# Kernel optimization log

Measured on AMD Instinct MI355X. Metric: run time of the kernel, lower is better.

Reference implementation:

```python
import jax, jax.numpy as jnp
import numpy as np

B = 65536
IN = 32 * 8      # input_size * n_dim
H = 256          # joint_hidden_size


def setup_inputs() -> dict:
    key = jax.random.key(0)
    ks = jax.random.split(key, 8)
    joint_h = jax.random.normal(ks[0], (B, H), dtype=jnp.float32)
    mgn_h = jax.random.normal(ks[1], (B, IN), dtype=jnp.float32)
    # xavier-uniform scale for W, plain normal for U (orthogonal in torch; any
    # dense matrix is fine for a numerical reference), zeros for biases.
    w_lim = float(np.sqrt(6.0 / (IN + H)))
    W_r = jax.random.uniform(ks[2], (IN, H), jnp.float32, -w_lim, w_lim)
    W_z = jax.random.uniform(ks[3], (IN, H), jnp.float32, -w_lim, w_lim)
    W_h = jax.random.uniform(ks[4], (IN, H), jnp.float32, -w_lim, w_lim)
    U_r = jax.random.normal(ks[5], (H, H), jnp.float32) / np.float32(np.sqrt(H))
    U_z = jax.random.normal(ks[6], (H, H), jnp.float32) / np.float32(np.sqrt(H))
    U_h = jax.random.normal(ks[7], (H, H), jnp.float32) / np.float32(np.sqrt(H))
    b_r = jnp.zeros((H,), jnp.float32)
    b_z = jnp.zeros((H,), jnp.float32)
    b_h = jnp.zeros((H,), jnp.float32)
    return {"joint_h": joint_h, "mgn_h": mgn_h,
            "W_r": W_r, "W_z": W_z, "W_h": W_h,
            "U_r": U_r, "U_z": U_z, "U_h": U_h,
            "b_r": b_r, "b_z": b_z, "b_h": b_h}


def reference(joint_h, mgn_h, W_r, W_z, W_h, U_r, U_z, U_h, b_r, b_z, b_h):
    # fuse the three input GEMMs and the two non-gated hidden GEMMs by
    # concatenating weights (same math as 6 separate mm's)
    W = jnp.concatenate([W_r, W_z, W_h], axis=1)        # [IN, 3H]
    U_rz = jnp.concatenate([U_r, U_z], axis=1)          # [H, 2H]
    x_proj = mgn_h @ W                                  # [B, 3H]
    h_proj = joint_h @ U_rz                             # [B, 2H]
    Hd = joint_h.shape[1]
    r = jax.nn.sigmoid(x_proj[:, :Hd] + h_proj[:, :Hd] + b_r)
    z = jax.nn.sigmoid(x_proj[:, Hd:2 * Hd] + h_proj[:, Hd:] + b_z)
    h_tilde = jnp.tanh(x_proj[:, 2 * Hd:] + (joint_h * r) @ U_h + b_h)
    return h_tilde + z * (joint_h - h_tilde)
```

## Files before the change

### kernel.cpp

```cpp
#include <hip/hip_runtime.h>

#define H     256
#define BM    128
#define NTHR  512
#define LDK2  264

typedef __attribute__((ext_vector_type(4))) float f32x4;
typedef __attribute__((ext_vector_type(8))) short bf16x8;

__device__ __forceinline__ ushort f2bf(float f) {
    union { float f; unsigned u; } v; v.f = f;
    unsigned u = v.u;
    unsigned r = (u + 0x7fffu + ((u >> 16) & 1u)) >> 16;
    return (ushort)r;
}
__device__ __forceinline__ float bf2f(ushort h) {
    union { unsigned u; float f; } v; v.u = ((unsigned)h) << 16;
    return v.f;
}
__device__ __forceinline__ float sigmoid_f(float x) {
    return __builtin_amdgcn_rcpf(1.0f + __expf(-x));
}
__device__ __forceinline__ float tanh_f(float x) {
    float ax = fabsf(x);
    float e  = __expf(-2.0f * ax);
    float t  = (1.0f - e) * __builtin_amdgcn_rcpf(1.0f + e);
    return copysignf(t, x);
}

__global__ void prep_w(const float* __restrict__ Wr, const float* __restrict__ Wz,
                       const float* __restrict__ Wh, const float* __restrict__ Ur,
                       const float* __restrict__ Uz, const float* __restrict__ Uh,
                       ushort* __restrict__ P)
{
    const int k  = blockIdx.x;
    const int kk = k & 255;
    const bool hi = k >= 256;
    for (int n = threadIdx.x; n < 768; n += 256) {
        float v;
        if (n < 256)      v = (hi ? Ur : Wr)[kk * 256 + n];
        else if (n < 512) v = (hi ? Uz : Wz)[kk * 256 + (n - 256)];
        else              v = (hi ? Uh : Wh)[kk * 256 + (n - 512)];
        P[(size_t)n * 512 + k] = f2bf(v);
    }
}

#define MFMA(a, b, c) __builtin_amdgcn_mfma_f32_16x16x32_bf16((a), (b), (c), 0, 0, 0)

#define RZ_STEP(SB, KOFF, K0) do {                                            \
    bf16x8 bR_[2], bZ_[2], af_[8];                                            \
    _Pragma("unroll") for (int j_ = 0; j_ < 2; ++j_) {                        \
        bR_[j_] = *(const bf16x8*)(pBr + (size_t)j_ * 16 * 512 + (KOFF) + (K0)); \
        bZ_[j_] = *(const bf16x8*)(pBz + (size_t)j_ * 16 * 512 + (KOFF) + (K0)); \
    }                                                                         \
    _Pragma("unroll") for (int i_ = 0; i_ < 8; ++i_)                          \
        af_[i_] = *(const bf16x8*)&SB[(i_ * 16 + l15) * LDK2 + (K0) + kq * 8];\
    _Pragma("unroll") for (int j_ = 0; j_ < 2; ++j_)                          \
    _Pragma("unroll") for (int i_ = 0; i_ < 8; ++i_) {                        \
        aR[i_][j_] = MFMA(af_[i_], bR_[j_], aR[i_][j_]);                      \
        aZ[i_][j_] = MFMA(af_[i_], bZ_[j_], aZ[i_][j_]);                      \
    }                                                                         \
} while (0)

#define H_STEP(SB, KOFF, K0) do {                                             \
    bf16x8 bH_[2], af_[8];                                                    \
    _Pragma("unroll") for (int j_ = 0; j_ < 2; ++j_)                          \
        bH_[j_] = *(const bf16x8*)(pBh + (size_t)j_ * 16 * 512 + (KOFF) + (K0)); \
    _Pragma("unroll") for (int i_ = 0; i_ < 8; ++i_)                          \
        af_[i_] = *(const bf16x8*)&SB[(i_ * 16 + l15) * LDK2 + (K0) + kq * 8];\
    _Pragma("unroll") for (int j_ = 0; j_ < 2; ++j_)                          \
    _Pragma("unroll") for (int i_ = 0; i_ < 8; ++i_)                          \
        aH[i_][j_] = MFMA(af_[i_], bH_[j_], aH[i_][j_]);                      \
} while (0)

#define LOADJ(JV, CI) do {                                                    \
    _Pragma("unroll") for (int i_ = 0; i_ < 4; ++i_) {                        \
        const int c_ = tid + ((CI) * 4 + i_) * NTHR;                          \
        JV[i_] = *(const f32x4*)(joint + (r0 + (c_ >> 6)) * H + (c_ & 63) * 4); \
    }                                                                         \
} while (0)

#define COMMITJ(JV, CI) do {                                                  \
    _Pragma("unroll") for (int i_ = 0; i_ < 4; ++i_) {                        \
        const int c_ = tid + ((CI) * 4 + i_) * NTHR;                          \
        ushort4 w_;                                                           \
        w_.x = f2bf(JV[i_][0]); w_.y = f2bf(JV[i_][1]);                       \
        w_.z = f2bf(JV[i_][2]); w_.w = f2bf(JV[i_][3]);                       \
        *(ushort4*)&sb1[(c_ >> 6) * LDK2 + (c_ & 63) * 4] = w_;               \
    }                                                                         \
} while (0)

__global__ __launch_bounds__(NTHR, 2)
void gru_main(const float* __restrict__ joint, const float* __restrict__ mgn,
              const ushort* __restrict__ P,
              const float* __restrict__ br_, const float* __restrict__ bz_,
              const float* __restrict__ bh_, float* __restrict__ out)
{
    __shared__ ushort sb0[BM * LDK2];
    __shared__ ushort sb1[BM * LDK2];

    const int tid  = threadIdx.x;
    const int wave = tid >> 6;
    const int lane = tid & 63;
    const int l15  = lane & 15;
    const int kq   = lane >> 4;
    const int colbase = wave * 32;
    const size_t r0 = (size_t)blockIdx.x * BM;

    const ushort* __restrict__ pBr = P + (size_t)(colbase + l15) * 512 + kq * 8;
    const ushort* __restrict__ pBz = pBr + (size_t)256 * 512;
    const ushort* __restrict__ pBh = pBr + (size_t)512 * 512;

    #pragma unroll
    for (int i = 0; i < 16; ++i) {
        const int c   = tid + i * NTHR;
        const int row = c >> 6;
        const int c4  = (c & 63) * 4;
        const f32x4 v = *(const f32x4*)(mgn + (r0 + row) * H + c4);
        ushort4 w;
        w.x = f2bf(v[0]); w.y = f2bf(v[1]); w.z = f2bf(v[2]); w.w = f2bf(v[3]);
        *(ushort4*)&sb0[row * LDK2 + c4] = w;
    }
    __syncthreads();

    f32x4 aR[8][2], aZ[8][2];
    #pragma unroll
    for (int i = 0; i < 8; ++i)
        #pragma unroll
        for (int j = 0; j < 2; ++j) {
            aR[i][j] = (f32x4){0.f, 0.f, 0.f, 0.f};
            aZ[i][j] = (f32x4){0.f, 0.f, 0.f, 0.f};
        }

    {
        f32x4 jvA[4], jvB[4];
        LOADJ(jvA, 0);
        RZ_STEP(sb0, 0, 0);   RZ_STEP(sb0, 0, 32);
        LOADJ(jvB, 1);
        RZ_STEP(sb0, 0, 64);  RZ_STEP(sb0, 0, 96);
        COMMITJ(jvA, 0); LOADJ(jvA, 2);
        RZ_STEP(sb0, 0, 128); RZ_STEP(sb0, 0, 160);
        COMMITJ(jvB, 1); LOADJ(jvB, 3);
        RZ_STEP(sb0, 0, 192); RZ_STEP(sb0, 0, 224);
        COMMITJ(jvA, 2);
        COMMITJ(jvB, 3);
    }
    __syncthreads();

    #pragma unroll 4
    for (int k0 = 0; k0 < 256; k0 += 32) RZ_STEP(sb1, 256, k0);
    __syncthreads();

    float br[2], bz[2], bh[2];
    #pragma unroll
    for (int j = 0; j < 2; ++j) {
        const int c = colbase + j * 16 + l15;
        br[j] = br_[c]; bz[j] = bz_[c]; bh[j] = bh_[c];
    }
    #pragma unroll
    for (int i = 0; i < 8; ++i)
        #pragma unroll
        for (int j = 0; j < 2; ++j)
            #pragma unroll
            for (int q = 0; q < 4; ++q) {
                const int row = i * 16 + kq * 4 + q;
                const int c   = colbase + j * 16 + l15;
                const float r = sigmoid_f(aR[i][j][q] + br[j]);
                const float hj = bf2f(sb1[row * LDK2 + c]);
                sb1[row * LDK2 + c] = f2bf(hj * r);
                aZ[i][j][q] = sigmoid_f(aZ[i][j][q] + bz[j]);
            }
    __syncthreads();

    f32x4 aH[8][2];
    #pragma unroll
    for (int i = 0; i < 8; ++i)
        #pragma unroll
        for (int j = 0; j < 2; ++j)
            aH[i][j] = (f32x4){0.f, 0.f, 0.f, 0.f};

    #pragma unroll 4
    for (int k0 = 0; k0 < 256; k0 += 32) H_STEP(sb1, 256, k0);
    #pragma unroll 4
    for (int k0 = 0; k0 < 256; k0 += 32) H_STEP(sb0, 0, k0);

    #pragma unroll
    for (int i = 0; i < 8; ++i)
        #pragma unroll
        for (int j = 0; j < 2; ++j)
            #pragma unroll
            for (int q = 0; q < 4; ++q) {
                const int row = i * 16 + kq * 4 + q;
                const int c   = colbase + j * 16 + l15;
                const float ht = tanh_f(aH[i][j][q] + bh[j]);
                const float z  = aZ[i][j][q];
                const float h  = joint[(r0 + row) * H + c];
                out[(r0 + row) * H + c] = ht + z * (h - ht);
            }
}

extern "C" void kernel_launch(void* const* d_in, const int* in_sizes, int n_in,
                              void* d_out, int out_size, void* d_ws, size_t ws_size,
                              hipStream_t stream)
{
    const float* joint = (const float*)d_in[0];
    const float* mgn   = (const float*)d_in[1];
    const float* Wr    = (const float*)d_in[2];
    const float* Wz    = (const float*)d_in[3];
    const float* Wh    = (const float*)d_in[4];
    const float* Ur    = (const float*)d_in[5];
    const float* Uz    = (const float*)d_in[6];
    const float* Uh    = (const float*)d_in[7];
    const float* br    = (const float*)d_in[8];
    const float* bz    = (const float*)d_in[9];
    const float* bh    = (const float*)d_in[10];

    ushort* P  = (ushort*)d_ws;
    float* out = (float*)d_out;

    prep_w<<<512, 256, 0, stream>>>(Wr, Wz, Wh, Ur, Uz, Uh, P);

    const int nrows = 65536;
    gru_main<<<nrows / BM, NTHR, 0, stream>>>(joint, mgn, P, br, bz, bh, out);
}
```

Measured before the change: 105.3 us.

## Split block into 16 waves with 2D row/column wave tiling

Doubles the block to 1024 threads and splits the 128-row tile across two wave groups of 64 rows each. Each wave now holds half as many accumulators, which lowers register pressure and gives more waves per CU to hide latency. In exchange, each B fragment fetched from global/L2 is reused over fewer MFMAs, so per-block weight traffic doubles. Larger blocks also make synchronisation coarser.

Result: slower. 137.3 us (+30.3%).

```diff
diff --git a/kernel.cpp b/kernel.cpp
--- a/kernel.cpp
+++ b/kernel.cpp
@@ -2,7 +2,7 @@
 
 #define H     256
 #define BM    128
-#define NTHR  512
+#define NTHR  1024
 #define LDK2  264
 
 typedef __attribute__((ext_vector_type(4))) float f32x4;
@@ -47,42 +47,50 @@
 
 #define MFMA(a, b, c) __builtin_amdgcn_mfma_f32_16x16x32_bf16((a), (b), (c), 0, 0, 0)
 
-#define RZ_STEP(SB, KOFF, K0) do {                                            \
-    bf16x8 bR_[2], bZ_[2], af_[8];                                            \
-    _Pragma("unroll") for (int j_ = 0; j_ < 2; ++j_) {                        \
-        bR_[j_] = *(const bf16x8*)(pBr + (size_t)j_ * 16 * 512 + (KOFF) + (K0)); \
-        bZ_[j_] = *(const bf16x8*)(pBz + (size_t)j_ * 16 * 512 + (KOFF) + (K0)); \
-    }                                                                         \
-    _Pragma("unroll") for (int i_ = 0; i_ < 8; ++i_)                          \
-        af_[i_] = *(const bf16x8*)&SB[(i_ * 16 + l15) * LDK2 + (K0) + kq * 8];\
-    _Pragma("unroll") for (int j_ = 0; j_ < 2; ++j_)                          \
-    _Pragma("unroll") for (int i_ = 0; i_ < 8; ++i_) {                        \
-        aR[i_][j_] = MFMA(af_[i_], bR_[j_], aR[i_][j_]);                      \
-        aZ[i_][j_] = MFMA(af_[i_], bZ_[j_], aZ[i_][j_]);                      \
-    }                                                                         \
-} while (0)
-
-#define H_STEP(SB, KOFF, K0) do {                                             \
-    bf16x8 bH_[2], af_[8];                                                    \
-    _Pragma("unroll") for (int j_ = 0; j_ < 2; ++j_)                          \
-        bH_[j_] = *(const bf16x8*)(pBh + (size_t)j_ * 16 * 512 + (KOFF) + (K0)); \
-    _Pragma("unroll") for (int i_ = 0; i_ < 8; ++i_)                          \
-        af_[i_] = *(const bf16x8*)&SB[(i_ * 16 + l15) * LDK2 + (K0) + kq * 8];\
-    _Pragma("unroll") for (int j_ = 0; j_ < 2; ++j_)                          \
-    _Pragma("unroll") for (int i_ = 0; i_ < 8; ++i_)                          \
-        aH[i_][j_] = MFMA(af_[i_], bH_[j_], aH[i_][j_]);                      \
+#define RZ_STEP(SB, K0, KOFF) do {                                            \
+    bf16x8 bR_[2], bZ_[2];                                                    \
+    bR_[0] = *(const bf16x8*)(pBr + (KOFF) + (K0));                           \
+    bR_[1] = *(const bf16x8*)(pBr + (size_t)16 * 512 + (KOFF) + (K0));        \
+    bZ_[0] = *(const bf16x8*)(pBz + (KOFF) + (K0));                           \
+    bZ_[1] = *(const bf16x8*)(pBz + (size_t)16 * 512 + (KOFF) + (K0));        \
+    _Pragma("unroll") for (int ip_ = 0; ip_ < 2; ++ip_) {                     \
+        bf16x8 a0_ = *(const bf16x8*)&SB[(rowbase + (ip_ * 2 + 0) * 16 + l15) * LDK2 + (K0) + kq * 8]; \
+        bf16x8 a1_ = *(const bf16x8*)&SB[(rowbase + (ip_ * 2 + 1) * 16 + l15) * LDK2 + (K0) + kq * 8]; \
+        aR[ip_ * 2 + 0][0] = MFMA(a0_, bR_[0], aR[ip_ * 2 + 0][0]);           \
+        aR[ip_ * 2 + 1][0] = MFMA(a1_, bR_[0], aR[ip_ * 2 + 1][0]);           \
+        aZ[ip_ * 2 + 0][0] = MFMA(a0_, bZ_[0], aZ[ip_ * 2 + 0][0]);           \
+        aZ[ip_ * 2 + 1][0] = MFMA(a1_, bZ_[0], aZ[ip_ * 2 + 1][0]);           \
+        aR[ip_ * 2 + 0][1] = MFMA(a0_, bR_[1], aR[ip_ * 2 + 0][1]);           \
+        aR[ip_ * 2 + 1][1] = MFMA(a1_, bR_[1], aR[ip_ * 2 + 1][1]);           \
+        aZ[ip_ * 2 + 0][1] = MFMA(a0_, bZ_[1], aZ[ip_ * 2 + 0][1]);           \
+        aZ[ip_ * 2 + 1][1] = MFMA(a1_, bZ_[1], aZ[ip_ * 2 + 1][1]);           \
+    }                                                                         \
+} while (0)
+
+#define H_STEP(SB, K0, KOFF) do {                                             \
+    bf16x8 bH_[2];                                                            \
+    bH_[0] = *(const bf16x8*)(pBh + (KOFF) + (K0));                           \
+    bH_[1] = *(const bf16x8*)(pBh + (size_t)16 * 512 + (KOFF) + (K0));        \
+    _Pragma("unroll") for (int ip_ = 0; ip_ < 2; ++ip_) {                     \
+        bf16x8 a0_ = *(const bf16x8*)&SB[(rowbase + (ip_ * 2 + 0) * 16 + l15) * LDK2 + (K0) + kq * 8]; \
+        bf16x8 a1_ = *(const bf16x8*)&SB[(rowbase + (ip_ * 2 + 1) * 16 + l15) * LDK2 + (K0) + kq * 8]; \
+        aH[ip_ * 2 + 0][0] = MFMA(a0_, bH_[0], aH[ip_ * 2 + 0][0]);           \
+        aH[ip_ * 2 + 1][0] = MFMA(a1_, bH_[0], aH[ip_ * 2 + 1][0]);           \
+        aH[ip_ * 2 + 0][1] = MFMA(a0_, bH_[1], aH[ip_ * 2 + 0][1]);           \
+        aH[ip_ * 2 + 1][1] = MFMA(a1_, bH_[1], aH[ip_ * 2 + 1][1]);           \
+    }                                                                         \
 } while (0)
 
 #define LOADJ(JV, CI) do {                                                    \
-    _Pragma("unroll") for (int i_ = 0; i_ < 4; ++i_) {                        \
-        const int c_ = tid + ((CI) * 4 + i_) * NTHR;                          \
+    _Pragma("unroll") for (int i_ = 0; i_ < 2; ++i_) {                        \
+        const int c_ = tid + ((CI) * 2 + i_) * NTHR;                          \
         JV[i_] = *(const f32x4*)(joint + (r0 + (c_ >> 6)) * H + (c_ & 63) * 4); \
     }                                                                         \
 } while (0)
 
 #define COMMITJ(JV, CI) do {                                                  \
-    _Pragma("unroll") for (int i_ = 0; i_ < 4; ++i_) {                        \
-        const int c_ = tid + ((CI) * 4 + i_) * NTHR;                          \
+    _Pragma("unroll") for (int i_ = 0; i_ < 2; ++i_) {                        \
+        const int c_ = tid + ((CI) * 2 + i_) * NTHR;                          \
         ushort4 w_;                                                           \
         w_.x = f2bf(JV[i_][0]); w_.y = f2bf(JV[i_][1]);                       \
         w_.z = f2bf(JV[i_][2]); w_.w = f2bf(JV[i_][3]);                       \
@@ -90,7 +98,7 @@
     }                                                                         \
 } while (0)
 
-__global__ __launch_bounds__(NTHR, 2)
+__global__ __launch_bounds__(NTHR, 4)
 void gru_main(const float* __restrict__ joint, const float* __restrict__ mgn,
               const ushort* __restrict__ P,
               const float* __restrict__ br_, const float* __restrict__ bz_,
@@ -104,7 +112,8 @@
     const int lane = tid & 63;
     const int l15  = lane & 15;
     const int kq   = lane >> 4;
-    const int colbase = wave * 32;
+    const int rowbase = (wave >> 3) * 64;
+    const int colbase = (wave & 7) * 32;
     const size_t r0 = (size_t)blockIdx.x * BM;
 
     const ushort* __restrict__ pBr = P + (size_t)(colbase + l15) * 512 + kq * 8;
@@ -112,7 +121,7 @@
     const ushort* __restrict__ pBh = pBr + (size_t)512 * 512;
 
     #pragma unroll
-    for (int i = 0; i < 16; ++i) {
+    for (int i = 0; i < 8; ++i) {
         const int c   = tid + i * NTHR;
         const int row = c >> 6;
         const int c4  = (c & 63) * 4;
@@ -123,9 +132,9 @@
     }
     __syncthreads();
 
-    f32x4 aR[8][2], aZ[8][2];
+    f32x4 aR[4][2], aZ[4][2];
     #pragma unroll
-    for (int i = 0; i < 8; ++i)
+    for (int i = 0; i < 4; ++i)
         #pragma unroll
         for (int j = 0; j < 2; ++j) {
             aR[i][j] = (f32x4){0.f, 0.f, 0.f, 0.f};
@@ -133,70 +142,76 @@
         }
 
     {
-        f32x4 jvA[4], jvB[4];
-        LOADJ(jvA, 0);
-        RZ_STEP(sb0, 0, 0);   RZ_STEP(sb0, 0, 32);
-        LOADJ(jvB, 1);
-        RZ_STEP(sb0, 0, 64);  RZ_STEP(sb0, 0, 96);
-        COMMITJ(jvA, 0); LOADJ(jvA, 2);
-        RZ_STEP(sb0, 0, 128); RZ_STEP(sb0, 0, 160);
-        COMMITJ(jvB, 1); LOADJ(jvB, 3);
-        RZ_STEP(sb0, 0, 192); RZ_STEP(sb0, 0, 224);
-        COMMITJ(jvA, 2);
-        COMMITJ(jvB, 3);
-    }
-    __syncthreads();
-
-    #pragma unroll 4
-    for (int k0 = 0; k0 < 256; k0 += 32) RZ_STEP(sb1, 256, k0);
-    __syncthreads();
-
-    float br[2], bz[2], bh[2];
+        f32x4 jv[2];
+        LOADJ(jv, 0);
+        RZ_STEP(sb0, 0, 0);   RZ_STEP(sb0, 32, 0);
+        COMMITJ(jv, 0);  LOADJ(jv, 1);
+        RZ_STEP(sb0, 64, 0);  RZ_STEP(sb0, 96, 0);
+        COMMITJ(jv, 1);  LOADJ(jv, 2);
+        RZ_STEP(sb0, 128, 0); RZ_STEP(sb0, 160, 0);
+        COMMITJ(jv, 2);  LOADJ(jv, 3);
+        RZ_STEP(sb0, 192, 0); RZ_STEP(sb0, 224, 0);
+        COMMITJ(jv, 3);
+    }
+    __syncthreads();
+
+    #pragma unroll 2
+    for (int k0 = 0; k0 < 256; k0 += 32) RZ_STEP(sb1, k0, 256);
+    __syncthreads();
+
+    {
+        float br[2], bz[2];
+        #pragma unroll
+        for (int j = 0; j < 2; ++j) {
+            const int c = colbase + j * 16 + l15;
+            br[j] = br_[c]; bz[j] = bz_[c];
+        }
+        #pragma unroll
+        for (int i = 0; i < 4; ++i)
+            #pragma unroll
+            for (int j = 0; j < 2; ++j)
+                #pragma unroll
+                for (int q = 0; q < 4; ++q) {
+                    const int row = rowbase + i * 16 + kq * 4 + q;
+                    const int c   = colbase + j * 16 + l15;
+                    const float r = sigmoid_f(aR[i][j][q] + br[j]);
+                    const float hj = bf2f(sb1[row * LDK2 + c]);
+                    sb1[row * LDK2 + c] = f2bf(hj * r);
+                    aZ[i][j][q] = sigmoid_f(aZ[i][j][q] + bz[j]);
+                }
+    }
+    __syncthreads();
+
+    f32x4 aH[4][2];
     #pragma unroll
-    for (int j = 0; j < 2; ++j) {
-        const int c = colbase + j * 16 + l15;
-        br[j] = br_[c]; bz[j] = bz_[c]; bh[j] = bh_[c];
-    }
-    #pragma unroll
-    for (int i = 0; i < 8; ++i)
-        #pragma unroll
-        for (int j = 0; j < 2; ++j)
-            #pragma unroll
-            for (int q = 0; q < 4; ++q) {
-                const int row = i * 16 + kq * 4 + q;
-                const int c   = colbase + j * 16 + l15;
-                const float r = sigmoid_f(aR[i][j][q] + br[j]);
-                const float hj = bf2f(sb1[row * LDK2 + c]);
-                sb1[row * LDK2 + c] = f2bf(hj * r);
-                aZ[i][j][q] = sigmoid_f(aZ[i][j][q] + bz[j]);
-            }
-    __syncthreads();
-
-    f32x4 aH[8][2];
-    #pragma unroll
-    for (int i = 0; i < 8; ++i)
+    for (int i = 0; i < 4; ++i)
         #pragma unroll
         for (int j = 0; j < 2; ++j)
             aH[i][j] = (f32x4){0.f, 0.f, 0.f, 0.f};
 
-    #pragma unroll 4
-    for (int k0 = 0; k0 < 256; k0 += 32) H_STEP(sb1, 256, k0);
-    #pragma unroll 4
-    for (int k0 = 0; k0 < 256; k0 += 32) H_STEP(sb0, 0, k0);
-
-    #pragma unroll
-    for (int i = 0; i < 8; ++i)
-        #pragma unroll
-        for (int j = 0; j < 2; ++j)
+    #pragma unroll 2
+    for (int k0 = 0; k0 < 256; k0 += 32) H_STEP(sb1, k0, 256);
+    #pragma unroll 2
+    for (int k0 = 0; k0 < 256; k0 += 32) H_STEP(sb0, k0, 0);
+
+    {
+        float bh[2];
+        #pragma unroll
+        for (int j = 0; j < 2; ++j) bh[j] = bh_[colbase + j * 16 + l15];
+        #pragma unroll
+        for (int i = 0; i < 4; ++i)
             #pragma unroll
-            for (int q = 0; q < 4; ++q) {
-                const int row = i * 16 + kq * 4 + q;
-                const int c   = colbase + j * 16 + l15;
-                const float ht = tanh_f(aH[i][j][q] + bh[j]);
-                const float z  = aZ[i][j][q];
-                const float h  = joint[(r0 + row) * H + c];
-                out[(r0 + row) * H + c] = ht + z * (h - ht);
-            }
+            for (int j = 0; j < 2; ++j)
+                #pragma unroll
+                for (int q = 0; q < 4; ++q) {
+                    const int row = rowbase + i * 16 + kq * 4 + q;
+                    const int c   = colbase + j * 16 + l15;
+                    const float ht = tanh_f(aH[i][j][q] + bh[j]);
+                    const float z  = aZ[i][j][q];
+                    const float h  = joint[(r0 + row) * H + c];
+                    out[(r0 + row) * H + c] = ht + z * (h - ht);
+                }
+    }
 }
 
 extern "C" void kernel_launch(void* const* d_in, const int* in_sizes, int n_in,
```

## Switch GRU kernel to 32x32 MFMA with pipelined staging and register-cached h,z

Applied to the files above, without the earlier changes.

Replaces the 16x16x32 bf16 MFMA tiling with 32x32x16 bf16 MFMA, so each wave covers 128 rows by 32 columns with fewer, larger fragments. It also streams the mgn tile into LDS in stages overlapped with the first r/z GEMM steps, and software-pipelines the B-operand global loads four steps ahead. The bf16 hidden state and z gate are packed into registers, which removes the global re-read of joint in the epilogue. The costs are higher register pressure, extra barriers between staging chunks, and using the bf16-rounded h in the final blend, which reduces accuracy.

After: 91.61 us. 1.15x faster.

```diff
diff --git a/kernel.cpp b/kernel.cpp
--- a/kernel.cpp
+++ b/kernel.cpp
@@ -5,8 +5,9 @@
 #define NTHR  512
 #define LDK2  264
 
-typedef __attribute__((ext_vector_type(4))) float f32x4;
-typedef __attribute__((ext_vector_type(8))) short bf16x8;
+typedef __attribute__((ext_vector_type(4)))  float f32x4;
+typedef __attribute__((ext_vector_type(16))) float f32x16;
+typedef __attribute__((ext_vector_type(8)))  short bf16x8;
 
 __device__ __forceinline__ ushort f2bf(float f) {
     union { float f; unsigned u; } v; v.f = f;
@@ -45,47 +46,69 @@
     }
 }
 
-#define MFMA(a, b, c) __builtin_amdgcn_mfma_f32_16x16x32_bf16((a), (b), (c), 0, 0, 0)
-
-#define RZ_STEP(SB, KOFF, K0) do {                                            \
-    bf16x8 bR_[2], bZ_[2], af_[8];                                            \
-    _Pragma("unroll") for (int j_ = 0; j_ < 2; ++j_) {                        \
-        bR_[j_] = *(const bf16x8*)(pBr + (size_t)j_ * 16 * 512 + (KOFF) + (K0)); \
-        bZ_[j_] = *(const bf16x8*)(pBz + (size_t)j_ * 16 * 512 + (KOFF) + (K0)); \
-    }                                                                         \
-    _Pragma("unroll") for (int i_ = 0; i_ < 8; ++i_)                          \
-        af_[i_] = *(const bf16x8*)&SB[(i_ * 16 + l15) * LDK2 + (K0) + kq * 8];\
-    _Pragma("unroll") for (int j_ = 0; j_ < 2; ++j_)                          \
-    _Pragma("unroll") for (int i_ = 0; i_ < 8; ++i_) {                        \
-        aR[i_][j_] = MFMA(af_[i_], bR_[j_], aR[i_][j_]);                      \
-        aZ[i_][j_] = MFMA(af_[i_], bZ_[j_], aZ[i_][j_]);                      \
-    }                                                                         \
-} while (0)
-
-#define H_STEP(SB, KOFF, K0) do {                                             \
-    bf16x8 bH_[2], af_[8];                                                    \
-    _Pragma("unroll") for (int j_ = 0; j_ < 2; ++j_)                          \
-        bH_[j_] = *(const bf16x8*)(pBh + (size_t)j_ * 16 * 512 + (KOFF) + (K0)); \
-    _Pragma("unroll") for (int i_ = 0; i_ < 8; ++i_)                          \
-        af_[i_] = *(const bf16x8*)&SB[(i_ * 16 + l15) * LDK2 + (K0) + kq * 8];\
-    _Pragma("unroll") for (int j_ = 0; j_ < 2; ++j_)                          \
-    _Pragma("unroll") for (int i_ = 0; i_ < 8; ++i_)                          \
-        aH[i_][j_] = MFMA(af_[i_], bH_[j_], aH[i_][j_]);                      \
-} while (0)
-
-#define LOADJ(JV, CI) do {                                                    \
-    _Pragma("unroll") for (int i_ = 0; i_ < 4; ++i_) {                        \
-        const int c_ = tid + ((CI) * 4 + i_) * NTHR;                          \
-        JV[i_] = *(const f32x4*)(joint + (r0 + (c_ >> 6)) * H + (c_ & 63) * 4); \
-    }                                                                         \
-} while (0)
-
-#define COMMITJ(JV, CI) do {                                                  \
-    _Pragma("unroll") for (int i_ = 0; i_ < 4; ++i_) {                        \
-        const int c_ = tid + ((CI) * 4 + i_) * NTHR;                          \
+#define MFMA32(a, b, c) __builtin_amdgcn_mfma_f32_32x32x16_bf16((a), (b), (c), 0, 0, 0)
+
+#define LBRZ(B, BR, BZ) do {                                                  \
+    const int ko_ = ((B) < 16) ? (B) * 16 : 256 + ((B) - 16) * 16;            \
+    BR = *(const bf16x8*)(pBr + ko_);                                         \
+    BZ = *(const bf16x8*)(pBz + ko_);                                         \
+} while (0)
+
+#define LBH(B, BH) do {                                                       \
+    const int ko_ = ((B) < 16) ? 256 + (B) * 16 : ((B) - 16) * 16;            \
+    BH = *(const bf16x8*)(pBh + ko_);                                         \
+} while (0)
+
+#define STEP1(SB, S16, BR, BZ) do {                                           \
+    const int kk_ = (S16) * 16;                                               \
+    bf16x8 af_[4];                                                            \
+    _Pragma("unroll") for (int rf_ = 0; rf_ < 4; ++rf_)                       \
+        af_[rf_] = *(const bf16x8*)&SB[(rf_ * 32 + l31) * LDK2 + kk_ + hi8];  \
+    _Pragma("unroll") for (int rf_ = 0; rf_ < 4; ++rf_) {                     \
+        aR[rf_] = MFMA32(af_[rf_], BR, aR[rf_]);                              \
+        aZ[rf_] = MFMA32(af_[rf_], BZ, aZ[rf_]);                              \
+    }                                                                         \
+} while (0)
+
+#define STEP2(SB, S16, BH) do {                                               \
+    const int kk_ = (S16) * 16;                                               \
+    bf16x8 af_[4];                                                            \
+    _Pragma("unroll") for (int rf_ = 0; rf_ < 4; ++rf_)                       \
+        af_[rf_] = *(const bf16x8*)&SB[(rf_ * 32 + l31) * LDK2 + kk_ + hi8];  \
+    _Pragma("unroll") for (int rf_ = 0; rf_ < 4; ++rf_)                       \
+        aH[rf_] = MFMA32(af_[rf_], BH, aH[rf_]);                              \
+} while (0)
+
+#define SLOADM(S) do {                                                        \
+    _Pragma("unroll") for (int j_ = 0; j_ < 4; ++j_) {                        \
+        const int u_ = j_ * NTHR + tid;                                       \
+        mv[j_] = *(const f32x4*)(mgn + (r0 + (u_ >> 4)) * H + ((S) * 16 + (u_ & 15)) * 4); \
+    }                                                                         \
+} while (0)
+
+#define SCOMMITM(S) do {                                                      \
+    _Pragma("unroll") for (int j_ = 0; j_ < 4; ++j_) {                        \
+        const int u_ = j_ * NTHR + tid;                                       \
         ushort4 w_;                                                           \
-        w_.x = f2bf(JV[i_][0]); w_.y = f2bf(JV[i_][1]);                       \
-        w_.z = f2bf(JV[i_][2]); w_.w = f2bf(JV[i_][3]);                       \
+        w_.x = f2bf(mv[j_][0]); w_.y = f2bf(mv[j_][1]);                       \
+        w_.z = f2bf(mv[j_][2]); w_.w = f2bf(mv[j_][3]);                       \
+        *(ushort4*)&sb0[(u_ >> 4) * LDK2 + ((S) * 16 + (u_ & 15)) * 4] = w_;  \
+    }                                                                         \
+} while (0)
+
+#define LOADJ(C) do {                                                         \
+    _Pragma("unroll") for (int i_ = 0; i_ < 2; ++i_) {                        \
+        const int c_ = tid + ((C) * 2 + i_) * NTHR;                           \
+        jv[i_] = *(const f32x4*)(joint + (r0 + (c_ >> 6)) * H + (c_ & 63) * 4); \
+    }                                                                         \
+} while (0)
+
+#define COMMITJ(C) do {                                                       \
+    _Pragma("unroll") for (int i_ = 0; i_ < 2; ++i_) {                        \
+        const int c_ = tid + ((C) * 2 + i_) * NTHR;                           \
+        ushort4 w_;                                                           \
+        w_.x = f2bf(jv[i_][0]); w_.y = f2bf(jv[i_][1]);                       \
+        w_.z = f2bf(jv[i_][2]); w_.w = f2bf(jv[i_][3]);                       \
         *(ushort4*)&sb1[(c_ >> 6) * LDK2 + (c_ & 63) * 4] = w_;               \
     }                                                                         \
 } while (0)
@@ -102,101 +125,158 @@
     const int tid  = threadIdx.x;
     const int wave = tid >> 6;
     const int lane = tid & 63;
-    const int l15  = lane & 15;
-    const int kq   = lane >> 4;
+    const int l31  = lane & 31;
+    const int hi8  = (lane >> 5) * 8;
+    const int hi4  = (lane >> 5) * 4;
     const int colbase = wave * 32;
+    const int col  = colbase + l31;
     const size_t r0 = (size_t)blockIdx.x * BM;
 
-    const ushort* __restrict__ pBr = P + (size_t)(colbase + l15) * 512 + kq * 8;
+    const ushort* __restrict__ pBr = P + (size_t)col * 512 + hi8;
     const ushort* __restrict__ pBz = pBr + (size_t)256 * 512;
     const ushort* __restrict__ pBh = pBr + (size_t)512 * 512;
 
+    f32x4 mv[4];
+    f32x4 jv[2];
+
+    SLOADM(0); SCOMMITM(0);
+    __syncthreads();
+
+    f32x16 aR[4], aZ[4];
     #pragma unroll
-    for (int i = 0; i < 16; ++i) {
-        const int c   = tid + i * NTHR;
-        const int row = c >> 6;
-        const int c4  = (c & 63) * 4;
-        const f32x4 v = *(const f32x4*)(mgn + (r0 + row) * H + c4);
-        ushort4 w;
-        w.x = f2bf(v[0]); w.y = f2bf(v[1]); w.z = f2bf(v[2]); w.w = f2bf(v[3]);
-        *(ushort4*)&sb0[row * LDK2 + c4] = w;
+    for (int rf = 0; rf < 4; ++rf)
+        #pragma unroll
+        for (int e = 0; e < 16; ++e) { aR[rf][e] = 0.f; aZ[rf][e] = 0.f; }
+
+    {
+        bf16x8 bRA, bZA, bRB, bZB, bRC, bZC, bRD, bZD;
+        LBRZ(0, bRA, bZA); LBRZ(1, bRB, bZB); LBRZ(2, bRC, bZC); LBRZ(3, bRD, bZD);
+        SLOADM(1); LOADJ(0);
+        STEP1(sb0, 0, bRA, bZA);  LBRZ(4, bRA, bZA);
+        STEP1(sb0, 1, bRB, bZB);  LBRZ(5, bRB, bZB);
+        STEP1(sb0, 2, bRC, bZC);  LBRZ(6, bRC, bZC);  COMMITJ(0); LOADJ(1); SCOMMITM(1);
+        STEP1(sb0, 3, bRD, bZD);  LBRZ(7, bRD, bZD);
+        __syncthreads();
+        SLOADM(2);
+        STEP1(sb0, 4, bRA, bZA);  LBRZ(8, bRA, bZA);  COMMITJ(1); LOADJ(2);
+        STEP1(sb0, 5, bRB, bZB);  LBRZ(9, bRB, bZB);
+        STEP1(sb0, 6, bRC, bZC);  LBRZ(10, bRC, bZC); COMMITJ(2); LOADJ(3); SCOMMITM(2);
+        STEP1(sb0, 7, bRD, bZD);  LBRZ(11, bRD, bZD);
+        __syncthreads();
+        SLOADM(3);
+        STEP1(sb0, 8, bRA, bZA);  LBRZ(12, bRA, bZA); COMMITJ(3); LOADJ(4);
+        STEP1(sb0, 9, bRB, bZB);  LBRZ(13, bRB, bZB);
+        STEP1(sb0, 10, bRC, bZC); LBRZ(14, bRC, bZC); COMMITJ(4); LOADJ(5); SCOMMITM(3);
+        STEP1(sb0, 11, bRD, bZD); LBRZ(15, bRD, bZD);
+        __syncthreads();
+        STEP1(sb0, 12, bRA, bZA); LBRZ(16, bRA, bZA); COMMITJ(5); LOADJ(6);
+        STEP1(sb0, 13, bRB, bZB); LBRZ(17, bRB, bZB);
+        STEP1(sb0, 14, bRC, bZC); LBRZ(18, bRC, bZC); COMMITJ(6); LOADJ(7);
+        STEP1(sb0, 15, bRD, bZD); LBRZ(19, bRD, bZD); COMMITJ(7);
+        __syncthreads();
+        STEP1(sb1, 0, bRA, bZA);  LBRZ(20, bRA, bZA);
+        STEP1(sb1, 1, bRB, bZB);  LBRZ(21, bRB, bZB);
+        STEP1(sb1, 2, bRC, bZC);  LBRZ(22, bRC, bZC);
+        STEP1(sb1, 3, bRD, bZD);  LBRZ(23, bRD, bZD);
+        STEP1(sb1, 4, bRA, bZA);  LBRZ(24, bRA, bZA);
+        STEP1(sb1, 5, bRB, bZB);  LBRZ(25, bRB, bZB);
+        STEP1(sb1, 6, bRC, bZC);  LBRZ(26, bRC, bZC);
+        STEP1(sb1, 7, bRD, bZD);  LBRZ(27, bRD, bZD);
+        STEP1(sb1, 8, bRA, bZA);  LBRZ(28, bRA, bZA);
+        STEP1(sb1, 9, bRB, bZB);  LBRZ(29, bRB, bZB);
+        STEP1(sb1, 10, bRC, bZC); LBRZ(30, bRC, bZC);
+        STEP1(sb1, 11, bRD, bZD); LBRZ(31, bRD, bZD);
+        STEP1(sb1, 12, bRA, bZA);
+        STEP1(sb1, 13, bRB, bZB);
+        STEP1(sb1, 14, bRC, bZC);
+        STEP1(sb1, 15, bRD, bZD);
     }
     __syncthreads();
 
-    f32x4 aR[8][2], aZ[8][2];
+    bf16x8 bHA, bHB, bHC, bHD;
+    LBH(0, bHA); LBH(1, bHB); LBH(2, bHC); LBH(3, bHD);
+
+    uint hs[32], zs[32];
+    {
+        const float brv = br_[col];
+        const float bzv = bz_[col];
+        #pragma unroll
+        for (int rf = 0; rf < 4; ++rf)
+            #pragma unroll
+            for (int m = 0; m < 16; m += 2) {
+                ushort hb[2], zb[2];
+                #pragma unroll
+                for (int e = 0; e < 2; ++e) {
+                    const int mm  = m + e;
+                    const int row = rf * 32 + (mm & 3) + 8 * (mm >> 2) + hi4;
+                    const int idx = row * LDK2 + col;
+                    const float r = sigmoid_f(aR[rf][mm] + brv);
+                    hb[e] = sb1[idx];
+                    sb1[idx] = f2bf(bf2f(hb[e]) * r);
+                    zb[e] = f2bf(sigmoid_f(aZ[rf][mm] + bzv));
+                }
+                hs[rf * 8 + (m >> 1)] = (uint)hb[0] | ((uint)hb[1] << 16);
+                zs[rf * 8 + (m >> 1)] = (uint)zb[0] | ((uint)zb[1] << 16);
+            }
+    }
+    __syncthreads();
+
+    f32x16 aH[4];
     #pragma unroll
-    for (int i = 0; i < 8; ++i)
+    for (int rf = 0; rf < 4; ++rf)
         #pragma unroll
-        for (int j = 0; j < 2; ++j) {
-            aR[i][j] = (f32x4){0.f, 0.f, 0.f, 0.f};
-            aZ[i][j] = (f32x4){0.f, 0.f, 0.f, 0.f};
-        }
+        for (int e = 0; e < 16; ++e) aH[rf][e] = 0.f;
 
     {
-        f32x4 jvA[4], jvB[4];
-        LOADJ(jvA, 0);
-        RZ_STEP(sb0, 0, 0);   RZ_STEP(sb0, 0, 32);
-        LOADJ(jvB, 1);
-        RZ_STEP(sb0, 0, 64);  RZ_STEP(sb0, 0, 96);
-        COMMITJ(jvA, 0); LOADJ(jvA, 2);
-        RZ_STEP(sb0, 0, 128); RZ_STEP(sb0, 0, 160);
-        COMMITJ(jvB, 1); LOADJ(jvB, 3);
-        RZ_STEP(sb0, 0, 192); RZ_STEP(sb0, 0, 224);
-        COMMITJ(jvA, 2);
-        COMMITJ(jvB, 3);
-    }
-    __syncthreads();
-
-    #pragma unroll 4
-    for (int k0 = 0; k0 < 256; k0 += 32) RZ_STEP(sb1, 256, k0);
-    __syncthreads();
-
-    float br[2], bz[2], bh[2];
-    #pragma unroll
-    for (int j = 0; j < 2; ++j) {
-        const int c = colbase + j * 16 + l15;
-        br[j] = br_[c]; bz[j] = bz_[c]; bh[j] = bh_[c];
-    }
-    #pragma unroll
-    for (int i = 0; i < 8; ++i)
+        STEP2(sb1, 0, bHA);  LBH(4, bHA);
+        STEP2(sb1, 1, bHB);  LBH(5, bHB);
+        STEP2(sb1, 2, bHC);  LBH(6, bHC);
+        STEP2(sb1, 3, bHD);  LBH(7, bHD);
+        STEP2(sb1, 4, bHA);  LBH(8, bHA);
+        STEP2(sb1, 5, bHB);  LBH(9, bHB);
+        STEP2(sb1, 6, bHC);  LBH(10, bHC);
+        STEP2(sb1, 7, bHD);  LBH(11, bHD);
+        STEP2(sb1, 8, bHA);  LBH(12, bHA);
+        STEP2(sb1, 9, bHB);  LBH(13, bHB);
+        STEP2(sb1, 10, bHC); LBH(14, bHC);
+        STEP2(sb1, 11, bHD); LBH(15, bHD);
+        STEP2(sb1, 12, bHA); LBH(16, bHA);
+        STEP2(sb1, 13, bHB); LBH(17, bHB);
+        STEP2(sb1, 14, bHC); LBH(18, bHC);
+        STEP2(sb1, 15, bHD); LBH(19, bHD);
+        STEP2(sb0, 0, bHA);  LBH(20, bHA);
+        STEP2(sb0, 1, bHB);  LBH(21, bHB);
+        STEP2(sb0, 2, bHC);  LBH(22, bHC);
+        STEP2(sb0, 3, bHD);  LBH(23, bHD);
+        STEP2(sb0, 4, bHA);  LBH(24, bHA);
+        STEP2(sb0, 5, bHB);  LBH(25, bHB);
+        STEP2(sb0, 6, bHC);  LBH(26, bHC);
+        STEP2(sb0, 7, bHD);  LBH(27, bHD);
+        STEP2(sb0, 8, bHA);  LBH(28, bHA);
+        STEP2(sb0, 9, bHB);  LBH(29, bHB);
+        STEP2(sb0, 10, bHC); LBH(30, bHC);
+        STEP2(sb0, 11, bHD); LBH(31, bHD);
+        STEP2(sb0, 12, bHA);
+        STEP2(sb0, 13, bHB);
+        STEP2(sb0, 14, bHC);
+        STEP2(sb0, 15, bHD);
+    }
+
+    {
+        const float bhv = bh_[col];
         #pragma unroll
-        for (int j = 0; j < 2; ++j)
+        for (int rf = 0; rf < 4; ++rf)
             #pragma unroll
-            for (int q = 0; q < 4; ++q) {
-                const int row = i * 16 + kq * 4 + q;
-                const int c   = colbase + j * 16 + l15;
-                const float r = sigmoid_f(aR[i][j][q] + br[j]);
-                const float hj = bf2f(sb1[row * LDK2 + c]);
-                sb1[row * LDK2 + c] = f2bf(hj * r);
-                aZ[i][j][q] = sigmoid_f(aZ[i][j][q] + bz[j]);
+            for (int m = 0; m < 16; ++m) {
+                const int row = rf * 32 + (m & 3) + 8 * (m >> 2) + hi4;
+                const float ht = tanh_f(aH[rf][m] + bhv);
+                const uint pk  = hs[rf * 8 + (m >> 1)];
+                const uint pz  = zs[rf * 8 + (m >> 1)];
+                const float h  = bf2f((ushort)(pk >> ((m & 1) * 16)));
+                const float z  = bf2f((ushort)(pz >> ((m & 1) * 16)));
+                out[(r0 + row) * H + col] = ht + z * (h - ht);
             }
-    __syncthreads();
-
-    f32x4 aH[8][2];
-    #pragma unroll
-    for (int i = 0; i < 8; ++i)
-        #pragma unroll
-        for (int j = 0; j < 2; ++j)
-            aH[i][j] = (f32x4){0.f, 0.f, 0.f, 0.f};
-
-    #pragma unroll 4
-    for (int k0 = 0; k0 < 256; k0 += 32) H_STEP(sb1, 256, k0);
-    #pragma unroll 4
-    for (int k0 = 0; k0 < 256; k0 += 32) H_STEP(sb0, 0, k0);
-
-    #pragma unroll
-    for (int i = 0; i < 8; ++i)
-        #pragma unroll
-        for (int j = 0; j < 2; ++j)
-            #pragma unroll
-            for (int q = 0; q < 4; ++q) {
-                const int row = i * 16 + kq * 4 + q;
-                const int c   = colbase + j * 16 + l15;
-                const float ht = tanh_f(aH[i][j][q] + bh[j]);
-                const float z  = aZ[i][j][q];
-                const float h  = joint[(r0 + row) * H + c];
-                out[(r0 + row) * H + c] = ht + z * (h - ht);
-            }
+    }
 }
 
 extern "C" void kernel_launch(void* const* d_in, const int* in_sizes, int n_in,
```
